# Optimization experiments

Hardware: AMD Instinct MI355X
Metric: run time of the kernel (lower is better)

## Reference

```python
import jax, jax.numpy as jnp
import numpy as np

B, SIZE, NF = 1024, 512, 128   # batch, hilbert.size = 2*256 orbitals, n_fermions
H, W = 32, 16                  # 2D FNO grid, H*W == SIZE
WIDTH, M1, M2 = 32, 4, 4       # FNO width and retained Fourier modes
TOTAL = SIZE * NF              # backflow output size (65536)


def setup_inputs() -> dict:
    key = jax.random.key(0)
    ks = jax.random.split(key, 10)
    s = 0.05
    return {
        "n": jax.random.randint(ks[0], (B, SIZE), 0, 2).astype(jnp.int32),
        "M_base": jax.random.normal(ks[1], (SIZE, NF), jnp.float32) * s,
        "lift_W": jax.random.normal(ks[2], (1, WIDTH), jnp.float32) * s,
        "lift_b": jnp.zeros((WIDTH,), jnp.float32),
        "spec_Wr": jax.random.normal(ks[3], (WIDTH, WIDTH, M1, M2), jnp.float32) * s,
        "spec_Wi": jax.random.normal(ks[4], (WIDTH, WIDTH, M1, M2), jnp.float32) * s,
        "pw_W": jax.random.normal(ks[5], (WIDTH, WIDTH), jnp.float32) * s,
        "pw_b": jnp.zeros((WIDTH,), jnp.float32),
        "proj_W": jax.random.normal(ks[6], (WIDTH, TOTAL), jnp.float32) * s,
        "proj_b": jnp.zeros((TOTAL,), jnp.float32),
    }


def _fno(nf, lift_W, lift_b, spec_Wr, spec_Wi, pw_W, pw_b, proj_W, proj_b):
    # nf: (B, SIZE) float occupations -> F_flat (B, TOTAL)
    g = nf.reshape(B, H, W, 1)
    h = g @ lift_W + lift_b                                   # (B,H,W,WIDTH) lifting
    xf = jnp.fft.rfft2(h, axes=(1, 2))                        # (B,H,W//2+1,WIDTH)
    Wc = (spec_Wr + 1j * spec_Wi).astype(jnp.complex64)       # (in,out,M1,M2)
    low = jnp.einsum("bxyi,ioxy->bxyo", xf[:, :M1, :M2, :], Wc)
    of = jnp.zeros_like(xf).at[:, :M1, :M2, :].set(low)       # keep only low modes
    hs = jnp.fft.irfft2(of, s=(H, W), axes=(1, 2))            # spectral conv output
    h2 = jnp.tanh(hs + h @ pw_W + pw_b)                       # spectral + pointwise
    pooled = h2.mean(axis=(1, 2))                             # (B,WIDTH)
    return pooled @ proj_W + proj_b                           # (B,TOTAL)


def reference(n, M_base, lift_W, lift_b, spec_Wr, spec_Wi, pw_W, pw_b, proj_W, proj_b):
    nf = n.astype(jnp.float32)
    F_flat = _fno(nf, lift_W, lift_b, spec_Wr, spec_Wi, pw_W, pw_b, proj_W, proj_b)
    # M(n) = M_base + F(n), per sample
    M = M_base[None, :, :] + F_flat.reshape(B, SIZE, NF)      # (B,SIZE,NF)
    # R = nonzero occupied-orbital indices (fixed size NF, fill 0)
    R = jax.vmap(lambda s: jnp.nonzero(s, size=NF, fill_value=0)[0])(n)  # (B,NF)
    A = jnp.take_along_axis(M, R[:, :, None], axis=1)         # (B,NF,NF) gathered rows
    sign, logabs = jnp.linalg.slogdet(A)
    # nkjax.logdet_cmplx: complex log-determinant of a real matrix
    return logabs.astype(jnp.complex64) + jnp.log(sign.astype(jnp.complex64))
```

## Files before the change

### kernel.cpp

```cpp
#include <hip/hip_runtime.h>
#include <math.h>

#ifndef M_PI
#define M_PI 3.14159265358979323846
#endif

#define BB 1024
#define SIZE 512
#define NF 128
#define WIDTH 32
#define TOTAL (SIZE*NF)

#define DPP_UMAX(x, ctrl, rmask) { \
    unsigned _t = (unsigned)__builtin_amdgcn_update_dpp(0, (int)(x), (ctrl), (rmask), 0xf, false); \
    if (_t > (x)) (x) = _t; }

__device__ __forceinline__ float readlanef(float x, int l) {
    return __int_as_float(__builtin_amdgcn_readlane(__float_as_int(x), l));
}

__device__ __forceinline__ float frcp_fast(float x) {
    float r = __builtin_amdgcn_rcpf(x);
    return r * (2.0f - x * r);
}

__global__ __launch_bounds__(256) void fno_pooled_kernel(
    const int*   __restrict__ n,
    const float* __restrict__ lift_W,
    const float* __restrict__ lift_b,
    const float* __restrict__ spec_Wr,
    const float* __restrict__ spec_Wi,
    const float* __restrict__ pw_W,
    const float* __restrict__ pw_b,
    float* __restrict__ pooled_g,
    signed char* __restrict__ pos_g)
{
    __shared__ float nf[SIZE];
    __shared__ float c32[32], s32[32];
    __shared__ float Gre[16], Gim[16];
    __shared__ float wsum[4][32];
    __shared__ float Arr[WIDTH][16], Aii[WIDTH][16];
    __shared__ float lowr[WIDTH][16], lowi[WIDTH][16];
    __shared__ float pwl[WIDTH], cb0[WIDTH];
    __shared__ float Brr[WIDTH], Bii[WIDTH];

    const int b = blockIdx.x;
    const int t = threadIdx.x;
    const int lane = t & 63;
    const int wave = t >> 6;

    if (t < 32) {
        float ang = (float)t * (2.0f * (float)M_PI / 32.0f);
        c32[t] = cosf(ang);
        s32[t] = sinf(ang);
    }
    for (int p = t; p < SIZE; p += 256) nf[p] = (float)n[b*SIZE + p];
    __syncthreads();

    if (wave == 0) {
        int base = 0;
        for (int c = 0; c < 8; ++c) {
            int p = c*64 + lane;
            bool occ = (nf[p] != 0.0f);
            unsigned long long mask = __ballot(occ);
            int prefix = __popcll(mask & ((1ull << lane) - 1ull));
            int pos = base + prefix;
            pos_g[(size_t)p*BB + b] = (occ && pos < NF) ? (signed char)pos : (signed char)-1;
            base += __popcll(mask);
        }
    }

    float gre[16], gim[16];
    #pragma unroll
    for (int m = 0; m < 16; ++m) { gre[m] = 0.f; gim[m] = 0.f; }
    for (int p = t; p < SIZE; p += 256) {
        float v = nf[p];
        int x = p >> 4, y = p & 15;
        #pragma unroll
        for (int kx = 0; kx < 4; ++kx) {
            #pragma unroll
            for (int ky = 0; ky < 4; ++ky) {
                int idx = (kx*x + 2*ky*y) & 31;
                gre[kx*4+ky] += v * c32[idx];
                gim[kx*4+ky] -= v * s32[idx];
            }
        }
    }
    #pragma unroll
    for (int m = 0; m < 16; ++m) {
        for (int off = 32; off > 0; off >>= 1) {
            gre[m] += __shfl_xor(gre[m], off, 64);
            gim[m] += __shfl_xor(gim[m], off, 64);
        }
    }
    if (lane == 0) {
        #pragma unroll
        for (int m = 0; m < 16; ++m) { wsum[wave][m] = gre[m]; wsum[wave][16+m] = gim[m]; }
    }
    __syncthreads();
    if (t < 32) {
        float s = wsum[0][t] + wsum[1][t] + wsum[2][t] + wsum[3][t];
        if (t < 16) Gre[t] = s; else Gim[t-16] = s;
    }

    for (int idx = t; idx < 512; idx += 256) {
        int o = idx >> 4, m = idx & 15;
        float ar = 0.f, ai = 0.f;
        for (int ii = 0; ii < WIDTH; ++ii) {
            float lw = lift_W[ii];
            ar += lw * spec_Wr[ii*512 + o*16 + m];
            ai += lw * spec_Wi[ii*512 + o*16 + m];
        }
        Arr[o][m] = ar; Aii[o][m] = ai;
    }
    if (t < 32) {
        float br = 0.f, bi = 0.f, pl = 0.f, cb = 0.f;
        for (int ii = 0; ii < WIDTH; ++ii) {
            float lb = lift_b[ii];
            br += lb * spec_Wr[ii*512 + t*16 + 0];
            bi += lb * spec_Wi[ii*512 + t*16 + 0];
            pl += lift_W[ii] * pw_W[ii*WIDTH + t];
            cb += lb * pw_W[ii*WIDTH + t];
        }
        Brr[t] = br; Bii[t] = bi;
        pwl[t] = pl;
        cb0[t] = cb + pw_b[t];
    }
    __syncthreads();

    for (int idx = t; idx < 512; idx += 256) {
        int o = idx >> 4, m = idx & 15;
        float gr = Gre[m], gi = Gim[m];
        float ar = Arr[o][m], ai = Aii[o][m];
        float lr = gr*ar - gi*ai;
        float li = gr*ai + gi*ar;
        if (m == 0) { lr += 512.f * Brr[o]; li += 512.f * Bii[o]; }
        lowr[o][m] = lr; lowi[o][m] = li;
    }
    __syncthreads();

    const int o  = t >> 3;
    const int xg = t & 7;
    const float plo = pwl[o], cbo = cb0[o];
    float acc = 0.f;
    const float inv32 = 1.0f/32.0f, inv16 = 1.0f/16.0f;
    for (int xi = 0; xi < 4; ++xi) {
        int x = xg*4 + xi;
        float Tre[4], Tim[4];
        #pragma unroll
        for (int ky = 0; ky < 4; ++ky) { Tre[ky] = 0.f; Tim[ky] = 0.f; }
        #pragma unroll
        for (int kx = 0; kx < 4; ++kx) {
            int idx = (kx*x) & 31;
            float c = c32[idx], s = s32[idx];
            #pragma unroll
            for (int ky = 0; ky < 4; ++ky) {
                float lr = lowr[o][kx*4+ky], li = lowi[o][kx*4+ky];
                Tre[ky] += lr*c - li*s;
                Tim[ky] += lr*s + li*c;
            }
        }
        #pragma unroll
        for (int ky = 0; ky < 4; ++ky) { Tre[ky] *= inv32; Tim[ky] *= inv32; }
        for (int y = 0; y < 16; ++y) {
            float hsv = Tre[0];
            #pragma unroll
            for (int ky = 1; ky < 4; ++ky) {
                int idx = (2*ky*y) & 31;
                hsv += 2.f*(Tre[ky]*c32[idx] - Tim[ky]*s32[idx]);
            }
            hsv *= inv16;
            float z = hsv + nf[x*16 + y]*plo + cbo;
            acc += tanhf(z);
        }
    }
    acc += __shfl_down(acc, 4, 8);
    acc += __shfl_down(acc, 2, 8);
    acc += __shfl_down(acc, 1, 8);
    if ((t & 7) == 0) pooled_g[b*WIDTH + o] = acc * (1.0f/512.0f);
}

__global__ __launch_bounds__(256) void build_kernel(
    const float* __restrict__ M_base,
    const float* __restrict__ proj_W,
    const float* __restrict__ proj_b,
    const float* __restrict__ pooled_g,
    const signed char* __restrict__ pos_g,
    float* __restrict__ A_ws)
{
    __shared__ float pooled_l[256*WIDTH];
    __shared__ signed char posl[256];

    const int r   = blockIdx.x >> 2;
    const int b0  = (blockIdx.x & 3) * 256;
    const int t   = threadIdx.x;
    const int j   = t & 127;
    const int sub = t >> 7;

    {
        const float4* src = (const float4*)(pooled_g + (size_t)b0*WIDTH);
        float4* dst = (float4*)pooled_l;
        for (int idx = t; idx < 256*WIDTH/4; idx += 256) dst[idx] = src[idx];
        if (t < 64) ((int*)posl)[t] = ((const int*)(pos_g + (size_t)r*BB + b0))[t];
    }

    float wj[WIDTH];
    #pragma unroll
    for (int o = 0; o < WIDTH; ++o) wj[o] = proj_W[(size_t)o*TOTAL + r*NF + j];
    const float base = M_base[r*NF + j] + proj_b[r*NF + j];
    __syncthreads();

    for (int bb = sub; bb < 256; bb += 2) {
        int pos = posl[bb];
        if (pos < 0) continue;
        const float4* pl4 = (const float4*)&pooled_l[bb*WIDTH];
        float4 p0 = pl4[0], p1 = pl4[1], p2 = pl4[2], p3 = pl4[3];
        float4 p4 = pl4[4], p5 = pl4[5], p6 = pl4[6], p7 = pl4[7];
        float acc = base;
        acc += p0.x*wj[0]  + p0.y*wj[1]  + p0.z*wj[2]  + p0.w*wj[3];
        acc += p1.x*wj[4]  + p1.y*wj[5]  + p1.z*wj[6]  + p1.w*wj[7];
        acc += p2.x*wj[8]  + p2.y*wj[9]  + p2.z*wj[10] + p2.w*wj[11];
        acc += p3.x*wj[12] + p3.y*wj[13] + p3.z*wj[14] + p3.w*wj[15];
        acc += p4.x*wj[16] + p4.y*wj[17] + p4.z*wj[18] + p4.w*wj[19];
        acc += p5.x*wj[20] + p5.y*wj[21] + p5.z*wj[22] + p5.w*wj[23];
        acc += p6.x*wj[24] + p6.y*wj[25] + p6.z*wj[26] + p6.w*wj[27];
        acc += p7.x*wj[28] + p7.y*wj[29] + p7.z*wj[30] + p7.w*wj[31];
        A_ws[((size_t)(b0+bb)*NF + pos)*NF + j] = acc;
    }
}

__global__ __launch_bounds__(512) void lu_kernel(
    const float* __restrict__ A_ws,
    float* __restrict__ out)
{
    __shared__ __align__(16) float pcolA[128*4];
    __shared__ __align__(16) float pcolB[128*4];
    __shared__ __align__(16) float Raw[8*128];
    __shared__ float pvbuf[128];
    __shared__ int   pivseq[128];

    const int t = threadIdx.x;
    const int l = t & 63;
    const int w = t >> 6;
    const int half = w & 1;
    const int q = w >> 1;
    const int i = l + 64*half;
    const int b = blockIdx.x;

    float4 Areg[8];
    {
        const float4* src = (const float4*)(A_ws + (size_t)b*(NF*NF) + i*NF + q*32);
        #pragma unroll
        for (int g = 0; g < 8; ++g) Areg[g] = src[g];
        if (q == 0) {
            *((float4*)&pcolA[i*4]) = Areg[0];
            *((float4*)&pcolB[i*4]) = Areg[1];
        }
    }
    bool done_i = false;
    bool done0 = false, done1 = false;
    __syncthreads();

    for (int p = 0; p < 16; ++p) {
        float4 a0v = *((const float4*)&pcolA[l*4]);
        float4 b0v = *((const float4*)&pcolB[l*4]);
        float4 a1v = *((const float4*)&pcolA[l*4 + 256]);
        float4 b1v = *((const float4*)&pcolB[l*4 + 256]);
        float v0[8] = { a0v.x,a0v.y,a0v.z,a0v.w, b0v.x,b0v.y,b0v.z,b0v.w };
        float v1[8] = { a1v.x,a1v.y,a1v.z,a1v.w, b1v.x,b1v.y,b1v.z,b1v.w };
        float lr0[8], lr1[8];
        int   prreg[8];

        #pragma unroll
        for (int k = 0; k < 8; ++k) {
            unsigned aa0 = __float_as_uint(v0[k]) & 0x7fffffffu;
            unsigned aa1 = __float_as_uint(v1[k]) & 0x7fffffffu;
            unsigned key0 = done0 ? 0u : ((aa0 & 0xffffff80u) | (unsigned)l);
            unsigned key1 = done1 ? 0u : ((aa1 & 0xffffff80u) | (unsigned)(l + 64));
            unsigned key = (key1 > key0) ? key1 : key0;
            DPP_UMAX(key, 0x111, 0xf);
            DPP_UMAX(key, 0x112, 0xf);
            DPP_UMAX(key, 0x114, 0xf);
            DPP_UMAX(key, 0x118, 0xf);
            DPP_UMAX(key, 0x142, 0xa);
            DPP_UMAX(key, 0x143, 0xc);
            const unsigned best = (unsigned)__builtin_amdgcn_readlane((int)key, 63);
            const int row = (int)(best & 127u);
            const int lw  = row & 63;
            const bool lowh = (row < 64);
            const float pv = lowh ? readlanef(v0[k], lw) : readlanef(v1[k], lw);
            prreg[k] = row;
            const float inv = frcp_fast(pv);
            float l0 = (done0 || row == l)      ? 0.f : v0[k] * inv;
            float l1 = (done1 || row == l + 64) ? 0.f : v1[k] * inv;
            lr0[k] = l0; lr1[k] = l1;
            if (row == l)      done0 = true;
            if (row == l + 64) done1 = true;
            #pragma unroll
            for (int j = 0; j < 8; ++j) if (j > k) {
                float ukj = lowh ? readlanef(v0[j], lw) : readlanef(v1[j], lw);
                v0[j] -= l0 * ukj;
                v1[j] -= l1 * ukj;
            }
            if (w == 0 && l == 0) { pivseq[8*p+k] = row; pvbuf[8*p+k] = pv; }
        }

        float cs[8];
        {
            float lm[8];
            #pragma unroll
            for (int s = 0; s < 8; ++s) lm[s] = half ? lr1[s] : lr0[s];
            #pragma unroll
            for (int s2 = 7; s2 >= 0; --s2) {
                float acc = -lm[s2];
                #pragma unroll
                for (int sp = 7; sp > 0; --sp) if (sp > s2) {
                    float Lt = (prreg[sp] < 64) ? readlanef(lr0[s2], prreg[sp])
                                                : readlanef(lr1[s2], prreg[sp] - 64);
                    acc -= cs[sp] * Lt;
                }
                cs[s2] = acc;
            }
        }

        int fp = -1;
        #pragma unroll
        for (int s = 0; s < 8; ++s) if (i == prreg[s]) fp = s;
        if (fp >= 0) {
            #pragma unroll
            for (int g = 0; g < 8; ++g)
                *((float4*)&Raw[fp*128 + (q*8 + g)*4]) = Areg[g];
        }
        __syncthreads();

        if (fp >= 0) {
            done_i = true;
        } else if (!done_i) {
            #pragma unroll
            for (int g = 0; g < 8; ++g) {
                const int G = q*8 + g;
                if (G > 2*p + 1) {
                    const int cbase = G*4;
                    float4 own = Areg[g];
                    #pragma unroll
                    for (int s = 0; s < 8; ++s) {
                        const float4 rv = *((const float4*)&Raw[s*128 + cbase]);
                        own.x += cs[s]*rv.x; own.y += cs[s]*rv.y;
                        own.z += cs[s]*rv.z; own.w += cs[s]*rv.w;
                    }
                    Areg[g] = own;
                    if (G == 2*p + 2) *((float4*)&pcolA[i*4]) = own;
                    if (G == 2*p + 3) *((float4*)&pcolB[i*4]) = own;
                }
            }
        }
        __syncthreads();
    }

    if (w == 0) {
        float d0 = pvbuf[l], d1 = pvbuf[l + 64];
        int   ps0 = pivseq[l], ps1 = pivseq[l + 64];
        float ls = logf(fabsf(d0)) + logf(fabsf(d1));
        int neg = ((d0 < 0.f) ? 1 : 0) ^ ((d1 < 0.f) ? 1 : 0);
        #pragma unroll
        for (int off = 32; off > 0; off >>= 1) {
            ls  += __shfl_xor(ls,  off, 64);
            neg ^= __shfl_xor(neg, off, 64);
        }
        unsigned long long vis0 = 0ull, vis1 = 0ull;
        int trans = 0;
        for (int k = 0; k < 128; ++k) {
            bool vk = (k < 64) ? ((vis0 >> k) & 1ull) : ((vis1 >> (k - 64)) & 1ull);
            if (!vk) {
                int j = k, len = 0;
                while (true) {
                    bool vj = (j < 64) ? ((vis0 >> j) & 1ull) : ((vis1 >> (j - 64)) & 1ull);
                    if (vj) break;
                    if (j < 64) vis0 |= (1ull << j); else vis1 |= (1ull << (j - 64));
                    j = (j < 64) ? __builtin_amdgcn_readlane(ps0, j)
                                 : __builtin_amdgcn_readlane(ps1, j - 64);
                    ++len;
                }
                trans += len - 1;
            }
        }
        if (l == 0) {
            int parity = (neg ^ (trans & 1)) & 1;
            out[b]      = ls;
            out[BB + b] = parity ? (float)M_PI : 0.0f;
        }
    }
}

extern "C" void kernel_launch(void* const* d_in, const int* in_sizes, int n_in,
                              void* d_out, int out_size, void* d_ws, size_t ws_size,
                              hipStream_t stream) {
    const int*   n       = (const int*)  d_in[0];
    const float* M_base  = (const float*)d_in[1];
    const float* lift_W  = (const float*)d_in[2];
    const float* lift_b  = (const float*)d_in[3];
    const float* spec_Wr = (const float*)d_in[4];
    const float* spec_Wi = (const float*)d_in[5];
    const float* pw_W    = (const float*)d_in[6];
    const float* pw_b    = (const float*)d_in[7];
    const float* proj_W  = (const float*)d_in[8];
    const float* proj_b  = (const float*)d_in[9];

    float*       pooled = (float*)d_ws;
    signed char* pos    = (signed char*)((char*)d_ws + 128*1024);
    float*       A_ws   = (float*)((char*)d_ws + (1 << 20));

    fno_pooled_kernel<<<BB, 256, 0, stream>>>(n, lift_W, lift_b, spec_Wr, spec_Wi,
                                              pw_W, pw_b, pooled, pos);
    build_kernel<<<SIZE*4, 256, 0, stream>>>(M_base, proj_W, proj_b, pooled, pos, A_ws);
    lu_kernel<<<BB, 512, 0, stream>>>(A_ws, (float*)d_out);
}
```

Before: 303.2 us.

## Double-buffer LU panel state to drop a barrier; loop batch tiles in build

The LU kernel now double-buffers the pivot column, pivot rows and elimination coefficients in shared memory. The next panel's columns are published before they are updated and then corrected at the start of the next step from the stored coefficients, which removes the second __syncthreads per step. Separately, build_kernel launches one block per orbital row and loops over four batch tiles, so each proj_W column slice is loaded into registers once instead of four times. The trade-offs are fewer blocks in build_kernel, meaning less parallelism, and extra LDS traffic and redundant FMAs for the deferred panel update.

```diff
diff --git a/kernel.cpp b/kernel.cpp
--- a/kernel.cpp
+++ b/kernel.cpp
@@ -191,41 +191,44 @@
     __shared__ float pooled_l[256*WIDTH];
     __shared__ signed char posl[256];
 
-    const int r   = blockIdx.x >> 2;
-    const int b0  = (blockIdx.x & 3) * 256;
+    const int r   = blockIdx.x;
     const int t   = threadIdx.x;
     const int j   = t & 127;
     const int sub = t >> 7;
-
-    {
-        const float4* src = (const float4*)(pooled_g + (size_t)b0*WIDTH);
-        float4* dst = (float4*)pooled_l;
-        for (int idx = t; idx < 256*WIDTH/4; idx += 256) dst[idx] = src[idx];
-        if (t < 64) ((int*)posl)[t] = ((const int*)(pos_g + (size_t)r*BB + b0))[t];
-    }
 
     float wj[WIDTH];
     #pragma unroll
     for (int o = 0; o < WIDTH; ++o) wj[o] = proj_W[(size_t)o*TOTAL + r*NF + j];
     const float base = M_base[r*NF + j] + proj_b[r*NF + j];
-    __syncthreads();
-
-    for (int bb = sub; bb < 256; bb += 2) {
-        int pos = posl[bb];
-        if (pos < 0) continue;
-        const float4* pl4 = (const float4*)&pooled_l[bb*WIDTH];
-        float4 p0 = pl4[0], p1 = pl4[1], p2 = pl4[2], p3 = pl4[3];
-        float4 p4 = pl4[4], p5 = pl4[5], p6 = pl4[6], p7 = pl4[7];
-        float acc = base;
-        acc += p0.x*wj[0]  + p0.y*wj[1]  + p0.z*wj[2]  + p0.w*wj[3];
-        acc += p1.x*wj[4]  + p1.y*wj[5]  + p1.z*wj[6]  + p1.w*wj[7];
-        acc += p2.x*wj[8]  + p2.y*wj[9]  + p2.z*wj[10] + p2.w*wj[11];
-        acc += p3.x*wj[12] + p3.y*wj[13] + p3.z*wj[14] + p3.w*wj[15];
-        acc += p4.x*wj[16] + p4.y*wj[17] + p4.z*wj[18] + p4.w*wj[19];
-        acc += p5.x*wj[20] + p5.y*wj[21] + p5.z*wj[22] + p5.w*wj[23];
-        acc += p6.x*wj[24] + p6.y*wj[25] + p6.z*wj[26] + p6.w*wj[27];
-        acc += p7.x*wj[28] + p7.y*wj[29] + p7.z*wj[30] + p7.w*wj[31];
-        A_ws[((size_t)(b0+bb)*NF + pos)*NF + j] = acc;
+
+    for (int tile = 0; tile < 4; ++tile) {
+        const int b0 = tile * 256;
+        __syncthreads();
+        {
+            const float4* src = (const float4*)(pooled_g + (size_t)b0*WIDTH);
+            float4* dst = (float4*)pooled_l;
+            for (int idx = t; idx < 256*WIDTH/4; idx += 256) dst[idx] = src[idx];
+            if (t < 64) ((int*)posl)[t] = ((const int*)(pos_g + (size_t)r*BB + b0))[t];
+        }
+        __syncthreads();
+
+        for (int bb = sub; bb < 256; bb += 2) {
+            int pos = posl[bb];
+            if (pos < 0) continue;
+            const float4* pl4 = (const float4*)&pooled_l[bb*WIDTH];
+            float4 p0 = pl4[0], p1 = pl4[1], p2 = pl4[2], p3 = pl4[3];
+            float4 p4 = pl4[4], p5 = pl4[5], p6 = pl4[6], p7 = pl4[7];
+            float acc = base;
+            acc += p0.x*wj[0]  + p0.y*wj[1]  + p0.z*wj[2]  + p0.w*wj[3];
+            acc += p1.x*wj[4]  + p1.y*wj[5]  + p1.z*wj[6]  + p1.w*wj[7];
+            acc += p2.x*wj[8]  + p2.y*wj[9]  + p2.z*wj[10] + p2.w*wj[11];
+            acc += p3.x*wj[12] + p3.y*wj[13] + p3.z*wj[14] + p3.w*wj[15];
+            acc += p4.x*wj[16] + p4.y*wj[17] + p4.z*wj[18] + p4.w*wj[19];
+            acc += p5.x*wj[20] + p5.y*wj[21] + p5.z*wj[22] + p5.w*wj[23];
+            acc += p6.x*wj[24] + p6.y*wj[25] + p6.z*wj[26] + p6.w*wj[27];
+            acc += p7.x*wj[28] + p7.y*wj[29] + p7.z*wj[30] + p7.w*wj[31];
+            A_ws[((size_t)(b0+bb)*NF + pos)*NF + j] = acc;
+        }
     }
 }
 
@@ -233,9 +236,11 @@
     const float* __restrict__ A_ws,
     float* __restrict__ out)
 {
-    __shared__ __align__(16) float pcolA[128*4];
-    __shared__ __align__(16) float pcolB[128*4];
-    __shared__ __align__(16) float Raw[8*128];
+    __shared__ __align__(16) float pcolA[2][128*4];
+    __shared__ __align__(16) float pcolB[2][128*4];
+    __shared__ __align__(16) float Raw[2][8*128];
+    __shared__ __align__(16) float coefA[2][128*4];
+    __shared__ __align__(16) float coefB[2][128*4];
     __shared__ float pvbuf[128];
     __shared__ int   pivseq[128];
 
@@ -253,8 +258,8 @@
         #pragma unroll
         for (int g = 0; g < 8; ++g) Areg[g] = src[g];
         if (q == 0) {
-            *((float4*)&pcolA[i*4]) = Areg[0];
-            *((float4*)&pcolB[i*4]) = Areg[1];
+            *((float4*)&pcolA[0][i*4]) = Areg[0];
+            *((float4*)&pcolB[0][i*4]) = Areg[1];
         }
     }
     bool done_i = false;
@@ -262,15 +267,37 @@
     __syncthreads();
 
     for (int p = 0; p < 16; ++p) {
-        float4 a0v = *((const float4*)&pcolA[l*4]);
-        float4 b0v = *((const float4*)&pcolB[l*4]);
-        float4 a1v = *((const float4*)&pcolA[l*4 + 256]);
-        float4 b1v = *((const float4*)&pcolB[l*4 + 256]);
+        const int cb = p & 1;
+
+        float4 a0v = *((const float4*)&pcolA[cb][l*4]);
+        float4 b0v = *((const float4*)&pcolB[cb][l*4]);
+        float4 a1v = *((const float4*)&pcolA[cb][l*4 + 256]);
+        float4 b1v = *((const float4*)&pcolB[cb][l*4 + 256]);
         float v0[8] = { a0v.x,a0v.y,a0v.z,a0v.w, b0v.x,b0v.y,b0v.z,b0v.w };
         float v1[8] = { a1v.x,a1v.y,a1v.z,a1v.w, b1v.x,b1v.y,b1v.z,b1v.w };
+
+        if (p > 0) {
+            const int pb = cb ^ 1;
+            const float4 c0a = *((const float4*)&coefA[pb][l*4]);
+            const float4 c0b = *((const float4*)&coefB[pb][l*4]);
+            const float4 c1a = *((const float4*)&coefA[pb][l*4 + 256]);
+            const float4 c1b = *((const float4*)&coefB[pb][l*4 + 256]);
+            const float c0[8] = { c0a.x,c0a.y,c0a.z,c0a.w, c0b.x,c0b.y,c0b.z,c0b.w };
+            const float c1[8] = { c1a.x,c1a.y,c1a.z,c1a.w, c1b.x,c1b.y,c1b.z,c1b.w };
+            const int G0 = 2*p, G1 = 2*p + 1;
+            #pragma unroll
+            for (int s = 0; s < 8; ++s) {
+                const float4 r0 = *((const float4*)&Raw[pb][s*128 + G0*4]);
+                const float4 r1 = *((const float4*)&Raw[pb][s*128 + G1*4]);
+                v0[0] += c0[s]*r0.x; v0[1] += c0[s]*r0.y; v0[2] += c0[s]*r0.z; v0[3] += c0[s]*r0.w;
+                v0[4] += c0[s]*r1.x; v0[5] += c0[s]*r1.y; v0[6] += c0[s]*r1.z; v0[7] += c0[s]*r1.w;
+                v1[0] += c1[s]*r0.x; v1[1] += c1[s]*r0.y; v1[2] += c1[s]*r0.z; v1[3] += c1[s]*r0.w;
+                v1[4] += c1[s]*r1.x; v1[5] += c1[s]*r1.y; v1[6] += c1[s]*r1.z; v1[7] += c1[s]*r1.w;
+            }
+        }
+
         float lr0[8], lr1[8];
         int   prreg[8];
-
         #pragma unroll
         for (int k = 0; k < 8; ++k) {
             unsigned aa0 = __float_as_uint(v0[k]) & 0x7fffffffu;
@@ -329,7 +356,25 @@
         if (fp >= 0) {
             #pragma unroll
             for (int g = 0; g < 8; ++g)
-                *((float4*)&Raw[fp*128 + (q*8 + g)*4]) = Areg[g];
+                *((float4*)&Raw[cb][fp*128 + (q*8 + g)*4]) = Areg[g];
+        }
+        if (q == 0) {
+            *((float4*)&coefA[cb][i*4]) = make_float4(cs[0], cs[1], cs[2], cs[3]);
+            *((float4*)&coefB[cb][i*4]) = make_float4(cs[4], cs[5], cs[6], cs[7]);
+        }
+        if (p < 15) {
+            const int nG0 = 2*p + 2;
+            if (q == (nG0 >> 3)) {
+                const int ge = nG0 & 7;
+                float4 ve = Areg[0], vo = Areg[1];
+                #pragma unroll
+                for (int g = 0; g < 8; ++g) {
+                    if (g == ge)     ve = Areg[g];
+                    if (g == ge + 1) vo = Areg[g];
+                }
+                *((float4*)&pcolA[cb ^ 1][i*4]) = ve;
+                *((float4*)&pcolB[cb ^ 1][i*4]) = vo;
+            }
         }
         __syncthreads();
 
@@ -344,17 +389,14 @@
                     float4 own = Areg[g];
                     #pragma unroll
                     for (int s = 0; s < 8; ++s) {
-                        const float4 rv = *((const float4*)&Raw[s*128 + cbase]);
+                        const float4 rv = *((const float4*)&Raw[cb][s*128 + cbase]);
                         own.x += cs[s]*rv.x; own.y += cs[s]*rv.y;
                         own.z += cs[s]*rv.z; own.w += cs[s]*rv.w;
                     }
                     Areg[g] = own;
-                    if (G == 2*p + 2) *((float4*)&pcolA[i*4]) = own;
-                    if (G == 2*p + 3) *((float4*)&pcolB[i*4]) = own;
                 }
             }
         }
-        __syncthreads();
     }
 
     if (w == 0) {
@@ -412,6 +454,6 @@
 
     fno_pooled_kernel<<<BB, 256, 0, stream>>>(n, lift_W, lift_b, spec_Wr, spec_Wi,
                                               pw_W, pw_b, pooled, pos);
-    build_kernel<<<SIZE*4, 256, 0, stream>>>(M_base, proj_W, proj_b, pooled, pos, A_ws);
+    build_kernel<<<SIZE, 256, 0, stream>>>(M_base, proj_W, proj_b, pooled, pos, A_ws);
     lu_kernel<<<BB, 512, 0, stream>>>(A_ws, (float*)d_out);
 }
```

After: 533.3 us. 1.76x slower.

## Interleave column groups across waves and pack LU updates into float2 vector math

Applied to the files above, without the earlier changes.

Column groups in the per-sample LU kernel are now assigned round-robin (G = q + 4*g) instead of contiguously per wave quarter. As columns are eliminated, the trailing-update work stays spread evenly across all four wave pairs rather than leaving early waves idle. The elimination and rank-8 update now use two-wide float vectors so the compiler can emit packed FMA instructions, and the Newton refinement step on the pivot reciprocal is dropped. The raw hardware reciprocal is slightly less accurate, which could affect the log-determinant's precision.

```diff
diff --git a/kernel.cpp b/kernel.cpp
--- a/kernel.cpp
+++ b/kernel.cpp
@@ -11,17 +11,14 @@
 #define WIDTH 32
 #define TOTAL (SIZE*NF)
 
+typedef float v2f __attribute__((ext_vector_type(2)));
+
 #define DPP_UMAX(x, ctrl, rmask) { \
     unsigned _t = (unsigned)__builtin_amdgcn_update_dpp(0, (int)(x), (ctrl), (rmask), 0xf, false); \
     if (_t > (x)) (x) = _t; }
 
 __device__ __forceinline__ float readlanef(float x, int l) {
     return __int_as_float(__builtin_amdgcn_readlane(__float_as_int(x), l));
-}
-
-__device__ __forceinline__ float frcp_fast(float x) {
-    float r = __builtin_amdgcn_rcpf(x);
-    return r * (2.0f - x * r);
 }
 
 __global__ __launch_bounds__(256) void fno_pooled_kernel(
@@ -249,13 +246,14 @@
 
     float4 Areg[8];
     {
-        const float4* src = (const float4*)(A_ws + (size_t)b*(NF*NF) + i*NF + q*32);
-        #pragma unroll
-        for (int g = 0; g < 8; ++g) Areg[g] = src[g];
+        const float* src = A_ws + (size_t)b*(NF*NF) + i*NF;
+        #pragma unroll
+        for (int g = 0; g < 8; ++g)
+            Areg[g] = *((const float4*)(src + (q + 4*g)*4));
         if (q == 0) {
             *((float4*)&pcolA[i*4]) = Areg[0];
-            *((float4*)&pcolB[i*4]) = Areg[1];
-        }
+        }
+        if (q == 1) *((float4*)&pcolB[i*4]) = Areg[0];
     }
     bool done_i = false;
     bool done0 = false, done1 = false;
@@ -266,15 +264,18 @@
         float4 b0v = *((const float4*)&pcolB[l*4]);
         float4 a1v = *((const float4*)&pcolA[l*4 + 256]);
         float4 b1v = *((const float4*)&pcolB[l*4 + 256]);
-        float v0[8] = { a0v.x,a0v.y,a0v.z,a0v.w, b0v.x,b0v.y,b0v.z,b0v.w };
-        float v1[8] = { a1v.x,a1v.y,a1v.z,a1v.w, b1v.x,b1v.y,b1v.z,b1v.w };
+        v2f vv[8];
+        vv[0] = (v2f){a0v.x, a1v.x}; vv[1] = (v2f){a0v.y, a1v.y};
+        vv[2] = (v2f){a0v.z, a1v.z}; vv[3] = (v2f){a0v.w, a1v.w};
+        vv[4] = (v2f){b0v.x, b1v.x}; vv[5] = (v2f){b0v.y, b1v.y};
+        vv[6] = (v2f){b0v.z, b1v.z}; vv[7] = (v2f){b0v.w, b1v.w};
         float lr0[8], lr1[8];
         int   prreg[8];
 
         #pragma unroll
         for (int k = 0; k < 8; ++k) {
-            unsigned aa0 = __float_as_uint(v0[k]) & 0x7fffffffu;
-            unsigned aa1 = __float_as_uint(v1[k]) & 0x7fffffffu;
+            unsigned aa0 = __float_as_uint(vv[k].x) & 0x7fffffffu;
+            unsigned aa1 = __float_as_uint(vv[k].y) & 0x7fffffffu;
             unsigned key0 = done0 ? 0u : ((aa0 & 0xffffff80u) | (unsigned)l);
             unsigned key1 = done1 ? 0u : ((aa1 & 0xffffff80u) | (unsigned)(l + 64));
             unsigned key = (key1 > key0) ? key1 : key0;
@@ -288,19 +289,19 @@
             const int row = (int)(best & 127u);
             const int lw  = row & 63;
             const bool lowh = (row < 64);
-            const float pv = lowh ? readlanef(v0[k], lw) : readlanef(v1[k], lw);
+            const float pv = lowh ? readlanef(vv[k].x, lw) : readlanef(vv[k].y, lw);
             prreg[k] = row;
-            const float inv = frcp_fast(pv);
-            float l0 = (done0 || row == l)      ? 0.f : v0[k] * inv;
-            float l1 = (done1 || row == l + 64) ? 0.f : v1[k] * inv;
+            const float inv = __builtin_amdgcn_rcpf(pv);
+            float l0 = (done0 || row == l)      ? 0.f : vv[k].x * inv;
+            float l1 = (done1 || row == l + 64) ? 0.f : vv[k].y * inv;
             lr0[k] = l0; lr1[k] = l1;
             if (row == l)      done0 = true;
             if (row == l + 64) done1 = true;
+            const v2f lv = (v2f){l0, l1};
             #pragma unroll
             for (int j = 0; j < 8; ++j) if (j > k) {
-                float ukj = lowh ? readlanef(v0[j], lw) : readlanef(v1[j], lw);
-                v0[j] -= l0 * ukj;
-                v1[j] -= l1 * ukj;
+                float ukj = lowh ? readlanef(vv[j].x, lw) : readlanef(vv[j].y, lw);
+                vv[j] -= lv * ukj;
             }
             if (w == 0 && l == 0) { pivseq[8*p+k] = row; pvbuf[8*p+k] = pv; }
         }
@@ -329,7 +330,7 @@
         if (fp >= 0) {
             #pragma unroll
             for (int g = 0; g < 8; ++g)
-                *((float4*)&Raw[fp*128 + (q*8 + g)*4]) = Areg[g];
+                *((float4*)&Raw[fp*128 + (q + 4*g)*4]) = Areg[g];
         }
         __syncthreads();
 
@@ -338,19 +339,20 @@
         } else if (!done_i) {
             #pragma unroll
             for (int g = 0; g < 8; ++g) {
-                const int G = q*8 + g;
+                const int G = q + 4*g;
                 if (G > 2*p + 1) {
                     const int cbase = G*4;
-                    float4 own = Areg[g];
+                    v2f o01 = (v2f){Areg[g].x, Areg[g].y};
+                    v2f o23 = (v2f){Areg[g].z, Areg[g].w};
                     #pragma unroll
                     for (int s = 0; s < 8; ++s) {
-                        const float4 rv = *((const float4*)&Raw[s*128 + cbase]);
-                        own.x += cs[s]*rv.x; own.y += cs[s]*rv.y;
-                        own.z += cs[s]*rv.z; own.w += cs[s]*rv.w;
+                        const v2f* rv2 = (const v2f*)&Raw[s*128 + cbase];
+                        o01 += rv2[0] * cs[s];
+                        o23 += rv2[1] * cs[s];
                     }
-                    Areg[g] = own;
-                    if (G == 2*p + 2) *((float4*)&pcolA[i*4]) = own;
-                    if (G == 2*p + 3) *((float4*)&pcolB[i*4]) = own;
+                    Areg[g] = make_float4(o01.x, o01.y, o23.x, o23.y);
+                    if (G == 2*p + 2) *((float4*)&pcolA[i*4]) = Areg[g];
+                    if (G == 2*p + 3) *((float4*)&pcolB[i*4]) = Areg[g];
                 }
             }
         }
```

After: 304.9 us. Within noise of the previous version (+0.5%).
